# Performance work log

Measured on AMD Instinct MI355X. Metric: run time of the kernel, lower is better.

Reference implementation:

```python
import jax, jax.numpy as jnp
import numpy as np

D_MODEL = 1024
N_HEAD = 16
D_K = D_MODEL // N_HEAD
B, S = 2, 2048


def setup_inputs() -> dict:
    key = jax.random.key(0)
    ks = jax.random.split(key, 12)
    sc = 1.0 / np.sqrt(D_MODEL)
    return {
        "q": jax.random.normal(ks[0], (B, S, D_MODEL), jnp.float32),
        "k": jax.random.normal(ks[1], (B, S, D_MODEL), jnp.float32),
        "v": jax.random.normal(ks[2], (B, S, D_MODEL), jnp.float32),
        "mask": jax.random.randint(ks[3], (B, S, S), 0, 2, jnp.int32),
        # learned params (torch Linear convention: y = x @ W + b with W pre-transposed)
        "wq": jax.random.normal(ks[4], (D_MODEL, D_MODEL), jnp.float32) * sc,
        "bq": jax.random.normal(ks[5], (D_MODEL,), jnp.float32) * sc,
        "wk": jax.random.normal(ks[6], (D_MODEL, D_MODEL), jnp.float32) * sc,  # no bias
        "wv": jax.random.normal(ks[7], (D_MODEL, D_MODEL), jnp.float32) * sc,
        "bv": jax.random.normal(ks[8], (D_MODEL,), jnp.float32) * sc,
        "wf": jax.random.normal(ks[9], (D_MODEL, D_MODEL), jnp.float32) * sc,
        "bf": jax.random.normal(ks[10], (D_MODEL,), jnp.float32) * sc,
    }


def reference(q, k, v, mask, wq, bq, wk, wv, bv, wf, bf):
    bs = q.shape[0]
    temperature = jnp.asarray(D_K ** 0.5, q.dtype)
    # projections -> [b, h, s, d_k]
    qh = (q @ wq + bq).reshape(bs, -1, N_HEAD, D_K).transpose(0, 2, 1, 3)
    kh = (k @ wk).reshape(bs, -1, N_HEAD, D_K).transpose(0, 2, 1, 3)
    vh = (v @ wv + bv).reshape(bs, -1, N_HEAD, D_K).transpose(0, 2, 1, 3)
    # scores [b, h, sq, sk]
    attn = jnp.einsum("bhqd,bhkd->bhqk", qh, kh) / temperature
    m0 = (mask[:, None, :, :] == 0)  # mask==0 -> masked out, broadcast over heads
    attn = jnp.where(m0, -jnp.inf, attn)
    attn = jax.nn.softmax(attn, axis=-1)
    attn = jnp.where(m0, 0.0, attn)
    out = jnp.einsum("bhqk,bhkd->bhqd", attn, vh)
    out = out.transpose(0, 2, 1, 3).reshape(bs, -1, D_MODEL)
    return out @ wf + bf  # dropout is identity in eval mode
```

## Files before the change

### kernel.cpp

```cpp
#include <hip/hip_runtime.h>

#define D_MODEL 1024
#define NHEAD   16
#define DK      64
#define BATCH   2
#define SEQ     2048

typedef __attribute__((ext_vector_type(8))) short bf16x8;
typedef __attribute__((ext_vector_type(4))) float f32x4;
typedef __attribute__((ext_vector_type(16))) float f32x16;
typedef __attribute__((ext_vector_type(4))) int i32x4;

#define QSCALE 0.18033688011f

__device__ __forceinline__ unsigned short f2b(float x) {
  unsigned u = __builtin_bit_cast(unsigned, x);
  u = (u + 0x7fffu + ((u >> 16) & 1u)) >> 16;
  return (unsigned short)u;
}
__device__ __forceinline__ unsigned short f2b_rhu(float x) {
  return (unsigned short)((__builtin_bit_cast(unsigned, x) + 0x8000u) >> 16);
}
__device__ __forceinline__ int pk2(float a, float b) {
  unsigned ua = __builtin_bit_cast(unsigned, a) + 0x8000u;
  unsigned ub = __builtin_bit_cast(unsigned, b) + 0x8000u;
  return (int)__builtin_amdgcn_perm(ub, ua, 0x07060302u);
}
__device__ __forceinline__ int pk2u(unsigned ua, unsigned ub) {
  return (int)__builtin_amdgcn_perm(ub + 0x8000u, ua + 0x8000u, 0x07060302u);
}

typedef const __attribute__((address_space(1))) void* gas_p;
typedef __attribute__((address_space(3))) void* las_p;
__device__ __forceinline__ void gll16(const void* g, void* l) {
  __builtin_amdgcn_global_load_lds((gas_p)g, (las_p)l, 16, 0, 0);
}

__device__ __forceinline__ f32x16 mfma32(bf16x8 a, bf16x8 b, f32x16 c) {
  return __builtin_amdgcn_mfma_f32_32x32x16_bf16(a, b, c, 0, 0, 0);
}

__global__ __launch_bounds__(256) void prep_kernel(
    const float* __restrict__ q, const float* __restrict__ k, const float* __restrict__ v,
    unsigned short* __restrict__ qb, unsigned short* __restrict__ kb,
    unsigned short* __restrict__ vb,
    const float* __restrict__ wq, const float* __restrict__ wk,
    const float* __restrict__ wv, const float* __restrict__ wf,
    unsigned short* __restrict__ wqt, unsigned short* __restrict__ wkt,
    unsigned short* __restrict__ wvt, unsigned short* __restrict__ wft,
    const int* __restrict__ mask, unsigned long long* __restrict__ mbits) {
  int bid = blockIdx.x, t = threadIdx.x;
  if (bid < 6144) {
    int by = bid >> 11, bx = bid & 2047;
    const float* src = by == 0 ? q : (by == 1 ? k : v);
    unsigned short* dst = by == 0 ? qb : (by == 1 ? kb : vb);
    size_t i = ((size_t)bx * 256 + t) * 8;
    float4 x0 = *(const float4*)&src[i];
    float4 x1 = *(const float4*)&src[i + 4];
    int4 w;
    w.x = pk2(x0.x, x0.y); w.y = pk2(x0.z, x0.w);
    w.z = pk2(x1.x, x1.y); w.w = pk2(x1.z, x1.w);
    *(int4*)&dst[i] = w;
  } else if (bid < 7168) {
    __shared__ float tile[64][65];
    int idx = bid - 6144;
    int bz = idx >> 8, by = (idx >> 4) & 15, bx = idx & 15;
    const float* w; unsigned short* wt;
    switch (bz) {
      case 0: w = wq; wt = wqt; break;
      case 1: w = wk; wt = wkt; break;
      case 2: w = wv; wt = wvt; break;
      default: w = wf; wt = wft; break;
    }
    int r0 = by * 64, c0 = bx * 64;
    for (int i = 0; i < 16; ++i) {
      int idx2 = t + i * 256; int r = idx2 >> 6, c = idx2 & 63;
      tile[r][c] = w[(size_t)(r0 + r) * D_MODEL + c0 + c];
    }
    __syncthreads();
    for (int i = 0; i < 16; ++i) {
      int idx2 = t + i * 256; int r = idx2 >> 6, c = idx2 & 63;
      wt[(size_t)(c0 + r) * D_MODEL + r0 + c] = f2b(tile[c][r]);
    }
  } else {
    int idx = bid - 7168;
    int lane = t & 63, wave = t >> 6;
    size_t base = ((size_t)idx * 4 + wave) * 256;
    unsigned long long b0 = __ballot(mask[base + lane] != 0);
    unsigned long long b1 = __ballot(mask[base + 64 + lane] != 0);
    unsigned long long b2 = __ballot(mask[base + 128 + lane] != 0);
    unsigned long long b3 = __ballot(mask[base + 192 + lane] != 0);
    if (lane == 0) {
      unsigned long long* p = &mbits[(size_t)idx * 16 + wave * 4];
      p[0] = b0; p[1] = b1; p[2] = b2; p[3] = b3;
    }
  }
}

__global__ __launch_bounds__(256) void gemm_qkv_kernel(
    const unsigned short* __restrict__ qb, const unsigned short* __restrict__ kb,
    const unsigned short* __restrict__ vb,
    const unsigned short* __restrict__ wqt, const unsigned short* __restrict__ wkt,
    const unsigned short* __restrict__ wvt,
    const float* __restrict__ bq, const float* __restrict__ bv,
    unsigned short* __restrict__ qh, unsigned short* __restrict__ kh,
    unsigned short* __restrict__ vt) {
  __shared__ unsigned short SB[16640];
  int bid = blockIdx.x;
  int xcd = bid & 7, slot = bid >> 3;
  int mi = slot & 3, zn = slot >> 2;
  int z = zn >> 3;
  int n0 = (zn & 7) * 128;
  int m0 = (mi * 8 + xcd) * 128;
  const unsigned short* A; const unsigned short* Bt;
  switch (z) {
    case 0:  A = qb; Bt = wqt; break;
    case 1:  A = kb; Bt = wkt; break;
    default: A = vb; Bt = wvt; break;
  }
  int t = threadIdx.x, lane = t & 63, wave = t >> 6;
  int l16 = lane & 15, quad = lane >> 4;
  int wm = (wave & 1) * 64, wn = (wave >> 1) * 64;
  f32x4 zero = {0.f, 0.f, 0.f, 0.f};
  f32x4 acc[4][4];
  for (int mt = 0; mt < 4; ++mt) for (int nt = 0; nt < 4; ++nt) acc[mt][nt] = zero;

  int drow = lane >> 2, dcol = (lane & 3) * 8;
  const unsigned short* asrc = A  + (size_t)(m0 + wave * 32 + drow) * D_MODEL + dcol;
  const unsigned short* bsrc = Bt + (size_t)(n0 + wave * 32 + drow) * D_MODEL + dcol;
  int dst = wave * 1024 + lane * 8;

#pragma unroll
  for (int g = 0; g < 2; ++g) {
    gll16(asrc + (size_t)(g * 16) * D_MODEL, &SB[dst + g * 512]);
    gll16(bsrc + (size_t)(g * 16) * D_MODEL, &SB[4096 + dst + g * 512]);
  }
  for (int it = 0; it < 32; ++it) {
    __syncthreads();
    if (it + 1 < 32) {
      int nb = ((it + 1) & 1) * 8192, kn = (it + 1) * 32;
#pragma unroll
      for (int g = 0; g < 2; ++g) {
        gll16(asrc + (size_t)(g * 16) * D_MODEL + kn, &SB[nb + dst + g * 512]);
        gll16(bsrc + (size_t)(g * 16) * D_MODEL + kn, &SB[nb + 4096 + dst + g * 512]);
      }
    }
    int cb = (it & 1) * 8192;
    bf16x8 a[4], b[4];
    for (int mt = 0; mt < 4; ++mt)
      a[mt] = *(const bf16x8*)&SB[cb + (wm + mt * 16 + l16) * 32 + quad * 8];
    for (int nt = 0; nt < 4; ++nt)
      b[nt] = *(const bf16x8*)&SB[cb + 4096 + (wn + nt * 16 + l16) * 32 + quad * 8];
    for (int mt = 0; mt < 4; ++mt)
      for (int nt = 0; nt < 4; ++nt)
        acc[mt][nt] = __builtin_amdgcn_mfma_f32_16x16x32_bf16(a[mt], b[nt], acc[mt][nt], 0, 0, 0);
  }

  if (z == 2) {
    __syncthreads();
    int qs = ((quad & 1) << 1) | (quad >> 1);
#pragma unroll
    for (int nt = 0; nt < 4; ++nt) {
      int col = wn + nt * 16 + l16;
      float bb = bv[n0 + col];
      for (int mt = 0; mt < 4; ++mt)
        for (int r = 0; r < 4; ++r)
          SB[col * 130 + wm + mt * 16 + qs * 4 + r] = f2b_rhu(acc[mt][nt][r] + bb);
    }
    __syncthreads();
    int c = t >> 1, hf = t & 1;
    int colg = n0 + c, hh = colg >> 6, dd = colg & 63;
    int b_ = m0 >> 11, sbase = m0 & (SEQ - 1);
    unsigned short* dstp = vt + (((size_t)(b_ * NHEAD + hh)) * DK + dd) * SEQ + sbase + hf * 64;
#pragma unroll
    for (int j = 0; j < 8; ++j)
      *(int4*)(dstp + j * 8) = *(const int4*)&SB[c * 130 + hf * 64 + j * 8];
  } else {
    __syncthreads();
#pragma unroll
    for (int nt = 0; nt < 4; ++nt) {
      int lcol = wn + nt * 16 + l16;
      float bb = (z == 0) ? bq[n0 + lcol] : 0.f;
      for (int mt = 0; mt < 4; ++mt)
        for (int r = 0; r < 4; ++r) {
          float val = acc[mt][nt][r] + bb;
          if (z == 0) val *= QSCALE;
          SB[(wm + mt * 16 + quad * 4 + r) * 130 + lcol] = f2b_rhu(val);
        }
    }
    __syncthreads();
    unsigned short* outp = (z == 0) ? qh : kh;
    int b_ = m0 >> 11, sbase = m0 & (SEQ - 1);
    int h0 = n0 >> 6, c = t & 7;
#pragma unroll
    for (int pass = 0; pass < 8; ++pass) {
      int rp = pass * 32 + (t >> 3);
      int srow = rp >> 1, part = rp & 1;
      unsigned short* dstp = outp +
          (((size_t)(b_ * NHEAD + h0 + part)) * SEQ + sbase + srow) * DK + c * 8;
      *(int4*)dstp = *(const int4*)&SB[srow * 130 + part * 64 + c * 8];
    }
  }
}

__global__ __launch_bounds__(256) void gemm_out_kernel(
    const unsigned short* __restrict__ A, const unsigned short* __restrict__ Bt,
    const float* __restrict__ bias, float* __restrict__ out) {
  __shared__ __align__(16) char SMEM[34816];
  unsigned short* As = (unsigned short*)SMEM;
  unsigned short* Bs = (unsigned short*)SMEM + 8192;
  float* OS = (float*)SMEM;
  int bid = blockIdx.x;
  int xcd = bid & 7, slot = bid >> 3;
  int mi = slot & 3, ni = slot >> 2;
  int m0 = (mi * 8 + xcd) * 128, n0 = ni * 64;
  int t = threadIdx.x, lane = t & 63, wave = t >> 6;
  int l16 = lane & 15, quad = lane >> 4;
  int wm = (wave & 1) * 64, wn = (wave >> 1) * 32;
  f32x4 zero = {0.f, 0.f, 0.f, 0.f};
  f32x4 acc[4][2];
  for (int mt = 0; mt < 4; ++mt) for (int nt = 0; nt < 2; ++nt) acc[mt][nt] = zero;

  int drow = lane >> 2, dcol = (lane & 3) * 8;
  const unsigned short* asrc = A  + (size_t)(m0 + wave * 32 + drow) * D_MODEL + dcol;
  const unsigned short* bsrc = Bt + (size_t)(n0 + (t >> 2)) * D_MODEL + (t & 3) * 8;
  int adst = wave * 1024 + lane * 8;
  int bdst = t * 8;

#pragma unroll
  for (int g = 0; g < 2; ++g)
    gll16(asrc + (size_t)(g * 16) * D_MODEL, &As[adst + g * 512]);
  gll16(bsrc, &Bs[bdst]);

  for (int it = 0; it < 32; ++it) {
    __syncthreads();
    if (it + 1 < 32) {
      int na = ((it + 1) & 1) * 4096, nbb = ((it + 1) & 1) * 2048;
      int kn = (it + 1) * 32;
#pragma unroll
      for (int g = 0; g < 2; ++g)
        gll16(asrc + (size_t)(g * 16) * D_MODEL + kn, &As[na + adst + g * 512]);
      gll16(bsrc + kn, &Bs[nbb + bdst]);
    }
    int ca = (it & 1) * 4096, cbb = (it & 1) * 2048;
    bf16x8 a[4], b[2];
    for (int mt = 0; mt < 4; ++mt)
      a[mt] = *(const bf16x8*)&As[ca + (wm + mt * 16 + l16) * 32 + quad * 8];
    for (int nt = 0; nt < 2; ++nt)
      b[nt] = *(const bf16x8*)&Bs[cbb + (wn + nt * 16 + l16) * 32 + quad * 8];
    for (int mt = 0; mt < 4; ++mt)
      for (int nt = 0; nt < 2; ++nt)
        acc[mt][nt] = __builtin_amdgcn_mfma_f32_16x16x32_bf16(a[mt], b[nt], acc[mt][nt], 0, 0, 0);
  }

  __syncthreads();
  {
    float b0 = bias[n0 + wn + l16];
    float b1 = bias[n0 + wn + 16 + l16];
#pragma unroll
    for (int mt = 0; mt < 4; ++mt)
      for (int nt = 0; nt < 2; ++nt)
        for (int r = 0; r < 4; ++r)
          OS[(wm + mt * 16 + quad * 4 + r) * 68 + wn + nt * 16 + l16] =
              acc[mt][nt][r] + (nt ? b1 : b0);
  }
  __syncthreads();
#pragma unroll
  for (int pass = 0; pass < 8; ++pass) {
    int row = pass * 16 + (t >> 4);
    int c4 = (t & 15) * 4;
    *(float4*)&out[(size_t)(m0 + row) * D_MODEL + n0 + c4] =
        *(const float4*)&OS[row * 68 + c4];
  }
}

__global__ __launch_bounds__(256, 2) void attn_kernel(
    const unsigned short* __restrict__ qh, const unsigned short* __restrict__ kh,
    const unsigned short* __restrict__ vt, const unsigned long long* __restrict__ mbits,
    unsigned short* __restrict__ attb) {
  __shared__ unsigned short Ks[16384];
  __shared__ unsigned short Vs[16384];
  int bid = blockIdx.x;
  int xcd = bid & 7, slot = bid >> 3;
  int bh_ = 4 * xcd + (slot >> 4);
  int qt = slot & 15;
  int b = bh_ >> 4, h = bh_ & 15;
  int t = threadIdx.x, lane = t & 63, wave = t >> 6;
  int l32 = lane & 31, hi = lane >> 5;
  size_t bh = (size_t)b * NHEAD + h;

  const unsigned short* Kg = kh + bh * SEQ * DK;
  const unsigned short* Vg = vt + bh * DK * SEQ;
  const unsigned long long* mrow = mbits + (size_t)b * SEQ * (SEQ / 64);
  int qrowb = qt * 128 + wave * 32;

  size_t mi0 = (size_t)(qrowb + l32) * (SEQ / 64);
  unsigned long long m0 = mrow[mi0];
  unsigned long long m1 = mrow[mi0 + 1];

  bf16x8 qf[4];
  {
    const unsigned short* Qg = qh + (bh * SEQ + (size_t)(qrowb + l32)) * DK;
#pragma unroll
    for (int step = 0; step < 4; ++step)
      qf[step] = *(const bf16x8*)&Qg[(step * 2 + hi) * 8];
  }

  int ksrow = t >> 3;
  int kschk = ((t & 7) ^ (ksrow & 7)) * 8;
  const unsigned short* ksrc = Kg + (size_t)ksrow * DK + kschk;
  int vsrow = t >> 4;
  int vschk = ((t & 15) ^ (vsrow & 15)) * 8;
  const unsigned short* vsrc = Vg + (size_t)vsrow * SEQ + vschk;
  int sdst = t * 8;

  int kx = l32 & 7;
  int kaddr[4];
#pragma unroll
  for (int step = 0; step < 4; ++step)
    kaddr[step] = l32 * 64 + (((step * 2 + hi) ^ kx) * 8);
  int vx = l32 & 15;

  bf16x8 ones8;
#pragma unroll
  for (int i = 0; i < 8; ++i) ones8[i] = (short)0x3F80;

  f32x16 zero16;
#pragma unroll
  for (int i = 0; i < 16; ++i) zero16[i] = 0.f;
  f32x16 accO0 = zero16, accO1 = zero16, accRS = zero16;

#pragma unroll
  for (int g = 0; g < 4; ++g) {
    gll16(ksrc + (size_t)(g * 32) * DK, &Ks[g * 2048 + sdst]);
    gll16(vsrc + (size_t)(g * 16) * SEQ, &Vs[g * 2048 + sdst]);
  }

  for (int tk = 0; tk < SEQ / 128; ++tk) {
    __syncthreads();
    unsigned long long n0m = m0, n1m = m1;
    if (tk + 1 < SEQ / 128) {
      int nb = ((tk + 1) & 1) * 8192;
      const unsigned short* kn = ksrc + (size_t)(tk + 1) * 128 * DK;
      const unsigned short* vn = vsrc + (tk + 1) * 128;
#pragma unroll
      for (int g = 0; g < 4; ++g) {
        gll16(kn + (size_t)(g * 32) * DK, &Ks[nb + g * 2048 + sdst]);
        gll16(vn + (size_t)(g * 16) * SEQ, &Vs[nb + g * 2048 + sdst]);
      }
      n0m = mrow[mi0 + 2 * (tk + 1)];
      n1m = mrow[mi0 + 2 * (tk + 1) + 1];
    }

    int cb = (tk & 1) * 8192;
#pragma unroll
    for (int kt = 0; kt < 4; ++kt) {
      f32x16 accS = zero16;
      __builtin_amdgcn_s_setprio(1);
#pragma unroll
      for (int step = 0; step < 4; ++step) {
        bf16x8 kf = *(const bf16x8*)&Ks[cb + kt * 2048 + kaddr[step]];
        accS = mfma32(kf, qf[step], accS);
      }
      __builtin_amdgcn_s_setprio(0);

      unsigned wk_ = (unsigned)(((kt < 2) ? m0 : m1) >> ((kt & 1) * 32));
      unsigned w = wk_ >> (4 * hi);
      unsigned pu[16];
#pragma unroll
      for (int r = 0; r < 16; ++r) {
        float pv = __builtin_amdgcn_exp2f(accS[r]);
        const int pos = (r & 3) + 8 * (r >> 2);
        int msk = ((int)(w << (31 - pos))) >> 31;
        pu[r] = __builtin_bit_cast(unsigned, pv) & (unsigned)msk;
      }
      i32x4 w0v = {pk2u(pu[0], pu[1]),  pk2u(pu[2], pu[3]),
                   pk2u(pu[4], pu[5]),  pk2u(pu[6], pu[7])};
      i32x4 w1v = {pk2u(pu[8], pu[9]),  pk2u(pu[10], pu[11]),
                   pk2u(pu[12], pu[13]), pk2u(pu[14], pu[15])};
      bf16x8 ap0 = __builtin_bit_cast(bf16x8, w0v);
      bf16x8 ap1 = __builtin_bit_cast(bf16x8, w1v);

      __builtin_amdgcn_s_setprio(1);
      accRS = mfma32(ap0, ones8, accRS);
      accRS = mfma32(ap1, ones8, accRS);
      {
        int c0 = ((kt * 4 + hi) ^ vx) * 8;
        int c1 = ((kt * 4 + 2 + hi) ^ vx) * 8;
        bf16x8 vf00 = *(const bf16x8*)&Vs[cb + l32 * 128 + c0];
        bf16x8 vf01 = *(const bf16x8*)&Vs[cb + 4096 + l32 * 128 + c0];
        bf16x8 vf10 = *(const bf16x8*)&Vs[cb + l32 * 128 + c1];
        bf16x8 vf11 = *(const bf16x8*)&Vs[cb + 4096 + l32 * 128 + c1];
        accO0 = mfma32(ap0, vf00, accO0);
        accO1 = mfma32(ap0, vf01, accO1);
        accO0 = mfma32(ap1, vf10, accO0);
        accO1 = mfma32(ap1, vf11, accO1);
      }
      __builtin_amdgcn_s_setprio(0);
    }
    m0 = n0m; m1 = n1m;
  }

#pragma unroll
  for (int r = 0; r < 16; ++r) {
    float sden = accRS[r];
    float inv = sden > 0.f ? 1.f / sden : 0.f;
    int qq = (r & 3) + 8 * (r >> 2) + 4 * hi;
    int row = qrowb + qq;
    size_t ob = ((size_t)b * SEQ + row) * D_MODEL + (size_t)h * DK + l32;
    attb[ob] = f2b_rhu(accO0[r] * inv);
    attb[ob + 32] = f2b_rhu(accO1[r] * inv);
  }
}

extern "C" void kernel_launch(void* const* d_in, const int* in_sizes, int n_in,
                              void* d_out, int out_size, void* d_ws, size_t ws_size,
                              hipStream_t stream) {
  (void)in_sizes; (void)n_in; (void)out_size; (void)ws_size;
  const float* q    = (const float*)d_in[0];
  const float* k    = (const float*)d_in[1];
  const float* v    = (const float*)d_in[2];
  const int*   mask = (const int*)d_in[3];
  const float* wq   = (const float*)d_in[4];
  const float* bq   = (const float*)d_in[5];
  const float* wk   = (const float*)d_in[6];
  const float* wv   = (const float*)d_in[7];
  const float* bv   = (const float*)d_in[8];
  const float* wf   = (const float*)d_in[9];
  const float* bf   = (const float*)d_in[10];

  char* ws = (char*)d_ws;
  unsigned short* wft  = (unsigned short*)(ws + 0);
  unsigned short* wqt  = (unsigned short*)(ws + 2097152);
  unsigned short* wkt  = (unsigned short*)(ws + 4194304);
  unsigned short* wvt  = (unsigned short*)(ws + 6291456);
  unsigned short* attb = (unsigned short*)(ws + 2097152);
  unsigned short* qhp  = (unsigned short*)(ws + 10485760);
  unsigned short* khp  = (unsigned short*)(ws + 18874368);
  unsigned short* vtp  = (unsigned short*)(ws + 27262976);
  unsigned long long* mbits = (unsigned long long*)(ws + 35651584);
  unsigned short* vb   = (unsigned short*)(ws + 36700160);
  unsigned short* qb   = (unsigned short*)d_out;
  unsigned short* kb   = (unsigned short*)d_out + 4194304;

  hipLaunchKernelGGL(prep_kernel, dim3(15360), dim3(256), 0, stream,
                     q, k, v, qb, kb, vb,
                     wq, wk, wv, wf, wqt, wkt, wvt, wft, mask, mbits);
  hipLaunchKernelGGL(gemm_qkv_kernel, dim3(768), dim3(256), 0, stream,
                     qb, kb, vb, wqt, wkt, wvt, bq, bv, qhp, khp, vtp);
  hipLaunchKernelGGL(attn_kernel, dim3(512), dim3(256), 0, stream,
                     qhp, khp, vtp, mbits, attb);
  hipLaunchKernelGGL(gemm_out_kernel, dim3(512), dim3(256), 0, stream,
                     attb, wft, bf, (float*)d_out);
}
```

Baseline: 248.6 us.

## Enlarge attention tiles to 256 rows/keys and software-pipeline QK^T

The attention kernel now uses 512-thread blocks covering 256 query rows, with 256-key K/V tiles double-buffered in 128KB of LDS, so half as many blocks are launched and each K/V load is shared by twice as many waves. The next 32-key QK^T MFMA block is computed before the exp/mask/PV work of the current one, which should hide the softmax latency behind matrix work. Mask words are loaded per tile instead of being prefetched one iteration ahead. The larger LDS footprint and block size may limit residency to one block per CU, and 256 blocks may underfill the GPU.

```diff
diff --git a/kernel.cpp b/kernel.cpp
--- a/kernel.cpp
+++ b/kernel.cpp
@@ -274,16 +274,16 @@
   }
 }
 
-__global__ __launch_bounds__(256, 2) void attn_kernel(
+__global__ __launch_bounds__(512, 2) void attn_kernel(
     const unsigned short* __restrict__ qh, const unsigned short* __restrict__ kh,
     const unsigned short* __restrict__ vt, const unsigned long long* __restrict__ mbits,
     unsigned short* __restrict__ attb) {
-  __shared__ unsigned short Ks[16384];
-  __shared__ unsigned short Vs[16384];
+  __shared__ unsigned short Ks[32768];
+  __shared__ unsigned short Vs[32768];
   int bid = blockIdx.x;
   int xcd = bid & 7, slot = bid >> 3;
-  int bh_ = 4 * xcd + (slot >> 4);
-  int qt = slot & 15;
+  int bh_ = 4 * xcd + (slot >> 3);
+  int qt = slot & 7;
   int b = bh_ >> 4, h = bh_ & 15;
   int t = threadIdx.x, lane = t & 63, wave = t >> 6;
   int l32 = lane & 31, hi = lane >> 5;
@@ -292,11 +292,7 @@
   const unsigned short* Kg = kh + bh * SEQ * DK;
   const unsigned short* Vg = vt + bh * DK * SEQ;
   const unsigned long long* mrow = mbits + (size_t)b * SEQ * (SEQ / 64);
-  int qrowb = qt * 128 + wave * 32;
-
-  size_t mi0 = (size_t)(qrowb + l32) * (SEQ / 64);
-  unsigned long long m0 = mrow[mi0];
-  unsigned long long m1 = mrow[mi0 + 1];
+  int qrowb = qt * 256 + wave * 32;
 
   bf16x8 qf[4];
   {
@@ -309,9 +305,7 @@
   int ksrow = t >> 3;
   int kschk = ((t & 7) ^ (ksrow & 7)) * 8;
   const unsigned short* ksrc = Kg + (size_t)ksrow * DK + kschk;
-  int vsrow = t >> 4;
-  int vschk = ((t & 15) ^ (vsrow & 15)) * 8;
-  const unsigned short* vsrc = Vg + (size_t)vsrow * SEQ + vschk;
+  int vrow0 = t >> 5;
   int sdst = t * 8;
 
   int kx = l32 & 7;
@@ -319,7 +313,8 @@
 #pragma unroll
   for (int step = 0; step < 4; ++step)
     kaddr[step] = l32 * 64 + (((step * 2 + hi) ^ kx) * 8);
-  int vx = l32 & 15;
+
+  size_t mi0 = (size_t)(qrowb + l32) * (SEQ / 64);
 
   bf16x8 ones8;
 #pragma unroll
@@ -332,44 +327,59 @@
 
 #pragma unroll
   for (int g = 0; g < 4; ++g) {
-    gll16(ksrc + (size_t)(g * 32) * DK, &Ks[g * 2048 + sdst]);
-    gll16(vsrc + (size_t)(g * 16) * SEQ, &Vs[g * 2048 + sdst]);
-  }
-
-  for (int tk = 0; tk < SEQ / 128; ++tk) {
-    __syncthreads();
-    unsigned long long n0m = m0, n1m = m1;
-    if (tk + 1 < SEQ / 128) {
-      int nb = ((tk + 1) & 1) * 8192;
-      const unsigned short* kn = ksrc + (size_t)(tk + 1) * 128 * DK;
-      const unsigned short* vn = vsrc + (tk + 1) * 128;
+    gll16(ksrc + (size_t)(g * 64) * DK, &Ks[g * 4096 + sdst]);
+    int vrow = g * 16 + vrow0;
+    int vch = ((t & 31) ^ (vrow & 31)) * 8;
+    gll16(Vg + (size_t)vrow * SEQ + vch, &Vs[g * 4096 + sdst]);
+  }
+
+  for (int tr = 0; tr < SEQ / 256; ++tr) {
+    __syncthreads();
+    if (tr + 1 < SEQ / 256) {
+      int nb = ((tr + 1) & 1) * 16384;
+      size_t k0 = (size_t)(tr + 1) * 256;
 #pragma unroll
       for (int g = 0; g < 4; ++g) {
-        gll16(kn + (size_t)(g * 32) * DK, &Ks[nb + g * 2048 + sdst]);
-        gll16(vn + (size_t)(g * 16) * SEQ, &Vs[nb + g * 2048 + sdst]);
+        gll16(ksrc + (k0 + g * 64) * DK, &Ks[nb + g * 4096 + sdst]);
+        int vrow = g * 16 + vrow0;
+        int vch = ((t & 31) ^ (vrow & 31)) * 8;
+        gll16(Vg + (size_t)vrow * SEQ + k0 + vch, &Vs[nb + g * 4096 + sdst]);
       }
-      n0m = mrow[mi0 + 2 * (tk + 1)];
-      n1m = mrow[mi0 + 2 * (tk + 1) + 1];
-    }
-
-    int cb = (tk & 1) * 8192;
-#pragma unroll
-    for (int kt = 0; kt < 4; ++kt) {
-      f32x16 accS = zero16;
-      __builtin_amdgcn_s_setprio(1);
-#pragma unroll
-      for (int step = 0; step < 4; ++step) {
-        bf16x8 kf = *(const bf16x8*)&Ks[cb + kt * 2048 + kaddr[step]];
-        accS = mfma32(kf, qf[step], accS);
+    }
+    unsigned long long mm[4];
+#pragma unroll
+    for (int j = 0; j < 4; ++j) mm[j] = mrow[mi0 + 4 * tr + j];
+
+    int cb = (tr & 1) * 16384;
+
+    f32x16 sA = zero16;
+    __builtin_amdgcn_s_setprio(1);
+#pragma unroll
+    for (int step = 0; step < 4; ++step) {
+      bf16x8 kf = *(const bf16x8*)&Ks[cb + kaddr[step]];
+      sA = mfma32(kf, qf[step], sA);
+    }
+    __builtin_amdgcn_s_setprio(0);
+
+#pragma unroll
+    for (int kt = 0; kt < 8; ++kt) {
+      f32x16 sB = zero16;
+      if (kt < 7) {
+        __builtin_amdgcn_s_setprio(1);
+#pragma unroll
+        for (int step = 0; step < 4; ++step) {
+          bf16x8 kf = *(const bf16x8*)&Ks[cb + (kt + 1) * 2048 + kaddr[step]];
+          sB = mfma32(kf, qf[step], sB);
+        }
+        __builtin_amdgcn_s_setprio(0);
       }
-      __builtin_amdgcn_s_setprio(0);
-
-      unsigned wk_ = (unsigned)(((kt < 2) ? m0 : m1) >> ((kt & 1) * 32));
-      unsigned w = wk_ >> (4 * hi);
+
+      unsigned w32 = (unsigned)(mm[kt >> 1] >> ((kt & 1) * 32));
+      unsigned w = w32 >> (4 * hi);
       unsigned pu[16];
 #pragma unroll
       for (int r = 0; r < 16; ++r) {
-        float pv = __builtin_amdgcn_exp2f(accS[r]);
+        float pv = __builtin_amdgcn_exp2f(sA[r]);
         const int pos = (r & 3) + 8 * (r >> 2);
         int msk = ((int)(w << (31 - pos))) >> 31;
         pu[r] = __builtin_bit_cast(unsigned, pv) & (unsigned)msk;
@@ -385,20 +395,21 @@
       accRS = mfma32(ap0, ones8, accRS);
       accRS = mfma32(ap1, ones8, accRS);
       {
-        int c0 = ((kt * 4 + hi) ^ vx) * 8;
-        int c1 = ((kt * 4 + 2 + hi) ^ vx) * 8;
-        bf16x8 vf00 = *(const bf16x8*)&Vs[cb + l32 * 128 + c0];
-        bf16x8 vf01 = *(const bf16x8*)&Vs[cb + 4096 + l32 * 128 + c0];
-        bf16x8 vf10 = *(const bf16x8*)&Vs[cb + l32 * 128 + c1];
-        bf16x8 vf11 = *(const bf16x8*)&Vs[cb + 4096 + l32 * 128 + c1];
+        int c0 = ((kt * 4 + hi) ^ l32) * 8;
+        int c1 = ((kt * 4 + 2 + hi) ^ l32) * 8;
+        bf16x8 vf00 = *(const bf16x8*)&Vs[cb + l32 * 256 + c0];
+        bf16x8 vf01 = *(const bf16x8*)&Vs[cb + 8192 + l32 * 256 + c0];
+        bf16x8 vf10 = *(const bf16x8*)&Vs[cb + l32 * 256 + c1];
+        bf16x8 vf11 = *(const bf16x8*)&Vs[cb + 8192 + l32 * 256 + c1];
         accO0 = mfma32(ap0, vf00, accO0);
         accO1 = mfma32(ap0, vf01, accO1);
         accO0 = mfma32(ap1, vf10, accO0);
         accO1 = mfma32(ap1, vf11, accO1);
       }
       __builtin_amdgcn_s_setprio(0);
-    }
-    m0 = n0m; m1 = n1m;
+
+      sA = sB;
+    }
   }
 
 #pragma unroll
@@ -448,7 +459,7 @@
                      wq, wk, wv, wf, wqt, wkt, wvt, wft, mask, mbits);
   hipLaunchKernelGGL(gemm_qkv_kernel, dim3(768), dim3(256), 0, stream,
                      qb, kb, vb, wqt, wkt, wvt, bq, bv, qhp, khp, vtp);
-  hipLaunchKernelGGL(attn_kernel, dim3(512), dim3(256), 0, stream,
+  hipLaunchKernelGGL(attn_kernel, dim3(256), dim3(512), 0, stream,
                      qhp, khp, vtp, mbits, attb);
   hipLaunchKernelGGL(gemm_out_kernel, dim3(512), dim3(256), 0, stream,
                      attb, wft, bf, (float*)d_out);
```

Result: no change. 247.7 us (-0.4%).
